# Kernel tuning notes

Hardware: AMD Instinct MI355X
Metric: run time of the kernel (lower is better)

## Reference

```python
import jax, jax.numpy as jnp
import numpy as np

BS, L = 2, 512
IN_CH, OUT_CH = 16, 16
HIDDEN = 8
KERNEL_SIZE = 5
SIM_SIZE = 5


def setup_inputs() -> dict:
    key = jax.random.key(0)
    ks = jax.random.split(key, 8)
    times = jax.random.uniform(ks[0], (BS, L), dtype=jnp.float32)
    features = jax.random.normal(ks[1], (BS, L, IN_CH), dtype=jnp.float32)
    max_true_len = L // (SIM_SIZE + 1)  # 85
    lengths = jax.random.randint(ks[2], (BS,), 1, max_true_len + 1).astype(jnp.int64)
    true_ids = jax.random.randint(ks[3], (BS, L), 0, 2).astype(bool)
    w1 = jax.random.normal(ks[4], (1, HIDDEN), dtype=jnp.float32) * 0.5
    b1 = jax.random.normal(ks[5], (HIDDEN,), dtype=jnp.float32) * 0.1
    w2 = jax.random.normal(ks[6], (HIDDEN, IN_CH * OUT_CH), dtype=jnp.float32) * 0.1
    b2 = jax.random.normal(ks[7], (IN_CH * OUT_CH,), dtype=jnp.float32) * 0.01
    return {"times": times, "features": features, "lengths": lengths,
            "true_ids": true_ids, "sim_size": SIM_SIZE,
            "w1": w1, "b1": b1, "w2": w2, "b2": b2}


def _dt_and_mask(times, lengths, true_ids, sim_size, kernel_size):
    Lm = times.shape[1]
    # S[b,l,j] = t_l - t_j
    S = times[:, :, None] - times[:, None, :]
    ones = jnp.ones((Lm, Lm), dtype=bool)
    # banded causal mask: j <= l and j >= l - (sim_size+1)*kernel_size + 1
    conv_mask = jnp.tril(ones) & jnp.triu(ones, k=-(sim_size + 1) * kernel_size + 1)
    # row l valid only while l <= (sim_size+1)*(length-1)
    len_mask = jnp.arange(Lm)[None, :, None] <= (sim_size + 1) * (lengths[:, None, None] - 1)
    dt_mask = true_ids[:, None, :] & conv_mask[None, :, :] & len_mask
    delta_times = jnp.where(dt_mask, S, jnp.zeros((), S.dtype))
    return delta_times, dt_mask


def reference(times, features, lengths, true_ids, sim_size, w1, b1, w2, b2):
    dt, dt_mask = _dt_and_mask(times, lengths, true_ids, sim_size, KERNEL_SIZE)
    # kernel MLP on scalar delta times: (bs,L,L,1) -> (bs,L,L,hidden) -> (bs,L,L,in*out)
    h = jax.nn.relu(dt[..., None] * w1[0] + b1)
    kv = h @ w2 + b2
    kv = jnp.where(dt_mask[..., None], kv, jnp.zeros((), kv.dtype))
    kv = kv.reshape(*kv.shape[:3], IN_CH, OUT_CH)  # (bs,L,L,in,out)
    # out[b,l,o] = sum_{j,i} features[b,j,i] * kv[b,l,j,i,o]
    out = jnp.einsum('bji,bljio->blo', features, kv)
    return out
```

## Files before the change

kernel.cpp:

```cpp
#include <hip/hip_runtime.h>

#define LSEQ 512
#define IN_CH 16
#define OUT_CH 16
#define HIDDEN 8
#define KSZ 5

__global__ __launch_bounds__(64) void contconv_kernel(
    const float* __restrict__ times,
    const float* __restrict__ feat,
    const int*   __restrict__ lengths,
    const int*   __restrict__ true_ids,
    const int*   __restrict__ sim_size_p,
    const float* __restrict__ w1,
    const float* __restrict__ b1,
    const float* __restrict__ w2,
    const float* __restrict__ b2,
    float*       __restrict__ out)
{
    const int bl = blockIdx.x;
    const int b  = bl >> 9;
    const int l  = bl & (LSEQ - 1);
    const int t  = threadIdx.x;
    const int o  = t & 15;
    const int jg = t >> 4;

    __shared__ float s_w2[HIDDEN * IN_CH * OUT_CH];
    __shared__ float s_b2[IN_CH * OUT_CH];
    for (int k = t; k < HIDDEN * IN_CH * OUT_CH; k += 64) s_w2[k] = w2[k];
    for (int k = t; k < IN_CH * OUT_CH; k += 64)          s_b2[k] = b2[k];

    const int sim  = sim_size_p[0];
    const int band = (sim + 1) * KSZ;
    const int len  = lengths[b];
    const bool rowvalid = (l <= (sim + 1) * (len - 1));

    float w1r[HIDDEN], b1r[HIDDEN];
#pragma unroll
    for (int h = 0; h < HIDDEN; ++h) { w1r[h] = w1[h]; b1r[h] = b1[h]; }

    __syncthreads();

    float acc = 0.0f;
    if (rowvalid) {
        const float tl = times[b * LSEQ + l];
        int jlo = l - band + 1;
        if (jlo < 0) jlo = 0;
        for (int j = jlo + jg; j <= l; j += 4) {
            if (true_ids[b * LSEQ + j] == 0) continue;
            const float dt = tl - times[b * LSEQ + j];

            float hv[HIDDEN];
#pragma unroll
            for (int h = 0; h < HIDDEN; ++h) {
                const float x = dt * w1r[h] + b1r[h];
                hv[h] = x > 0.0f ? x : 0.0f;
            }

            float q[HIDDEN];
#pragma unroll
            for (int h = 0; h < HIDDEN; ++h) q[h] = 0.0f;
            float fb = 0.0f;

            const float* fj = feat + (b * LSEQ + j) * IN_CH;
#pragma unroll
            for (int i = 0; i < IN_CH; ++i) {
                const float f = fj[i];
                fb += f * s_b2[i * OUT_CH + o];
#pragma unroll
                for (int h = 0; h < HIDDEN; ++h)
                    q[h] += f * s_w2[h * (IN_CH * OUT_CH) + i * OUT_CH + o];
            }

            float contrib = fb;
#pragma unroll
            for (int h = 0; h < HIDDEN; ++h) contrib += hv[h] * q[h];
            acc += contrib;
        }
    }

    acc += __shfl_xor(acc, 16, 64);
    acc += __shfl_xor(acc, 32, 64);

    if (t < 16) out[(b * LSEQ + l) * OUT_CH + o] = acc;
}

extern "C" void kernel_launch(void* const* d_in, const int* in_sizes, int n_in,
                              void* d_out, int out_size, void* d_ws, size_t ws_size,
                              hipStream_t stream) {
    const float* times    = (const float*)d_in[0];
    const float* feat     = (const float*)d_in[1];
    const int*   lengths  = (const int*)  d_in[2];
    const int*   true_ids = (const int*)  d_in[3];
    const int*   sim      = (const int*)  d_in[4];
    const float* w1       = (const float*)d_in[5];
    const float* b1       = (const float*)d_in[6];
    const float* w2       = (const float*)d_in[7];
    const float* b2       = (const float*)d_in[8];
    float* out = (float*)d_out;

    const int BS = in_sizes[0] / LSEQ;
    contconv_kernel<<<BS * LSEQ, 64, 0, stream>>>(
        times, feat, lengths, true_ids, sim, w1, b1, w2, b2, out);
}
```

Measured before the change: 80.29 us.

## Precompute per-position feature-weight projections in a separate pass, reuse across band rows

A first kernel computes, for every position j, the contraction of features with w2 and b2 (q[h,o] and the bias term), masked by true_ids, and writes them to workspace. The banded kernel then only evaluates the hidden ReLU per pair and takes a dot product with the precomputed vectors. Before, that contraction was recomputed for every (l,j) pair, up to 30 times per j. The cost is a second launch plus a workspace round-trip of 12 floats per (j,o).

```diff
diff --git a/kernel.cpp b/kernel.cpp
--- a/kernel.cpp
+++ b/kernel.cpp
@@ -5,17 +5,67 @@
 #define OUT_CH 16
 #define HIDDEN 8
 #define KSZ 5
+#define PSTRIDE 12
 
-__global__ __launch_bounds__(64) void contconv_kernel(
+__global__ __launch_bounds__(256) void phase1_kernel(
+    const float* __restrict__ feat,
+    const int*   __restrict__ true_ids,
+    const float* __restrict__ w2,
+    const float* __restrict__ b2,
+    float*       __restrict__ P)
+{
+    const int t  = threadIdx.x;
+    const int o  = t & 15;
+    const int jl = t >> 4;
+    const int bj = blockIdx.x * 16 + jl;
+
+    __shared__ float s_w2t[OUT_CH * IN_CH * HIDDEN];
+    __shared__ float s_b2[IN_CH * OUT_CH];
+    for (int k = t; k < HIDDEN * IN_CH * OUT_CH; k += 256) {
+        const int h = k >> 8, rem = k & 255, i = rem >> 4, oo = rem & 15;
+        s_w2t[(oo * IN_CH + i) * HIDDEN + h] = w2[k];
+    }
+    s_b2[t] = b2[t];
+    __syncthreads();
+
+    const float4* f4 = (const float4*)(feat + bj * IN_CH);
+    float f[IN_CH];
+    {
+        float4 a0 = f4[0], a1 = f4[1], a2 = f4[2], a3 = f4[3];
+        f[0]=a0.x; f[1]=a0.y; f[2]=a0.z; f[3]=a0.w;
+        f[4]=a1.x; f[5]=a1.y; f[6]=a1.z; f[7]=a1.w;
+        f[8]=a2.x; f[9]=a2.y; f[10]=a2.z; f[11]=a2.w;
+        f[12]=a3.x; f[13]=a3.y; f[14]=a3.z; f[15]=a3.w;
+    }
+    const float m = (true_ids[bj] != 0) ? 1.0f : 0.0f;
+
+    float q[HIDDEN];
+#pragma unroll
+    for (int h = 0; h < HIDDEN; ++h) q[h] = 0.0f;
+    float F = 0.0f;
+
+#pragma unroll
+    for (int i = 0; i < IN_CH; ++i) {
+        const float* wrow = &s_w2t[(o * IN_CH + i) * HIDDEN];
+        const float fi = f[i];
+#pragma unroll
+        for (int h = 0; h < HIDDEN; ++h) q[h] += fi * wrow[h];
+        F += fi * s_b2[i * OUT_CH + o];
+    }
+
+    float4* dst = (float4*)(P + (bj * OUT_CH + o) * PSTRIDE);
+    dst[0] = make_float4(q[0]*m, q[1]*m, q[2]*m, q[3]*m);
+    dst[1] = make_float4(q[4]*m, q[5]*m, q[6]*m, q[7]*m);
+    dst[2] = make_float4(F*m, 0.0f, 0.0f, 0.0f);
+}
+
+__global__ __launch_bounds__(64) void phase2_kernel(
     const float* __restrict__ times,
-    const float* __restrict__ feat,
     const int*   __restrict__ lengths,
-    const int*   __restrict__ true_ids,
     const int*   __restrict__ sim_size_p,
     const float* __restrict__ w1,
     const float* __restrict__ b1,
-    const float* __restrict__ w2,
-    const float* __restrict__ b2,
+    const float* __restrict__ P,
     float*       __restrict__ out)
 {
     const int bl = blockIdx.x;
@@ -25,57 +75,35 @@
     const int o  = t & 15;
     const int jg = t >> 4;
 
-    __shared__ float s_w2[HIDDEN * IN_CH * OUT_CH];
-    __shared__ float s_b2[IN_CH * OUT_CH];
-    for (int k = t; k < HIDDEN * IN_CH * OUT_CH; k += 64) s_w2[k] = w2[k];
-    for (int k = t; k < IN_CH * OUT_CH; k += 64)          s_b2[k] = b2[k];
-
-    const int sim  = sim_size_p[0];
-    const int band = (sim + 1) * KSZ;
-    const int len  = lengths[b];
-    const bool rowvalid = (l <= (sim + 1) * (len - 1));
-
-    float w1r[HIDDEN], b1r[HIDDEN];
-#pragma unroll
-    for (int h = 0; h < HIDDEN; ++h) { w1r[h] = w1[h]; b1r[h] = b1[h]; }
-
-    __syncthreads();
+    const int sim = sim_size_p[0];
+    const int len = lengths[b];
 
     float acc = 0.0f;
-    if (rowvalid) {
+    if (l <= (sim + 1) * (len - 1)) {
+        float w1r[HIDDEN], b1r[HIDDEN];
+#pragma unroll
+        for (int h = 0; h < HIDDEN; ++h) { w1r[h] = w1[h]; b1r[h] = b1[h]; }
+
         const float tl = times[b * LSEQ + l];
-        int jlo = l - band + 1;
+        int jlo = l - (sim + 1) * KSZ + 1;
         if (jlo < 0) jlo = 0;
+
         for (int j = jlo + jg; j <= l; j += 4) {
-            if (true_ids[b * LSEQ + j] == 0) continue;
             const float dt = tl - times[b * LSEQ + j];
+            const float4* p4 = (const float4*)(P + ((b * LSEQ + j) * OUT_CH + o) * PSTRIDE);
+            const float4 g0 = p4[0];
+            const float4 g1 = p4[1];
+            const float4 g2 = p4[2];
 
-            float hv[HIDDEN];
-#pragma unroll
-            for (int h = 0; h < HIDDEN; ++h) {
-                const float x = dt * w1r[h] + b1r[h];
-                hv[h] = x > 0.0f ? x : 0.0f;
-            }
-
-            float q[HIDDEN];
-#pragma unroll
-            for (int h = 0; h < HIDDEN; ++h) q[h] = 0.0f;
-            float fb = 0.0f;
-
-            const float* fj = feat + (b * LSEQ + j) * IN_CH;
-#pragma unroll
-            for (int i = 0; i < IN_CH; ++i) {
-                const float f = fj[i];
-                fb += f * s_b2[i * OUT_CH + o];
-#pragma unroll
-                for (int h = 0; h < HIDDEN; ++h)
-                    q[h] += f * s_w2[h * (IN_CH * OUT_CH) + i * OUT_CH + o];
-            }
-
-            float contrib = fb;
-#pragma unroll
-            for (int h = 0; h < HIDDEN; ++h) contrib += hv[h] * q[h];
-            acc += contrib;
+            acc += g2.x;
+            acc += fmaxf(dt * w1r[0] + b1r[0], 0.0f) * g0.x;
+            acc += fmaxf(dt * w1r[1] + b1r[1], 0.0f) * g0.y;
+            acc += fmaxf(dt * w1r[2] + b1r[2], 0.0f) * g0.z;
+            acc += fmaxf(dt * w1r[3] + b1r[3], 0.0f) * g0.w;
+            acc += fmaxf(dt * w1r[4] + b1r[4], 0.0f) * g1.x;
+            acc += fmaxf(dt * w1r[5] + b1r[5], 0.0f) * g1.y;
+            acc += fmaxf(dt * w1r[6] + b1r[6], 0.0f) * g1.z;
+            acc += fmaxf(dt * w1r[7] + b1r[7], 0.0f) * g1.w;
         }
     }
 
@@ -98,8 +126,10 @@
     const float* w2       = (const float*)d_in[7];
     const float* b2       = (const float*)d_in[8];
     float* out = (float*)d_out;
+    float* P   = (float*)d_ws;
 
     const int BS = in_sizes[0] / LSEQ;
-    contconv_kernel<<<BS * LSEQ, 64, 0, stream>>>(
-        times, feat, lengths, true_ids, sim, w1, b1, w2, b2, out);
+
+    phase1_kernel<<<BS * LSEQ / 16, 256, 0, stream>>>(feat, true_ids, w2, b2, P);
+    phase2_kernel<<<BS * LSEQ, 64, 0, stream>>>(times, lengths, sim, w1, b1, P, out);
 }
```

Measured after the change: 79.22 us. About the same (-1.3%).
